# Kernel tuning notes

Hardware: AMD Instinct MI355X
Metric: run time of the kernel (lower is better)

The kernel has to match this reference:

```python
import jax, jax.numpy as jnp
from jax import lax
import numpy as np


def _lstm(x, h0, c0, Wih, Whh, bih, bhh):
    """Single-layer batch-first LSTM, PyTorch gate order (i, f, g, o).
    x: [B, T, I]; h0, c0: [B, H]. Returns (outputs [B, T, H], h_n [B, H], c_n [B, H])."""
    # Precompute input projections for all timesteps in one GEMM.
    xg = jnp.einsum('bti,gi->btg', x, Wih) + (bih + bhh)  # [B, T, 4H]
    H = h0.shape[-1]

    def step(carry, xt):
        h, c = carry
        gates = xt + h @ Whh.T  # [B, 4H]
        i, f, g, o = jnp.split(gates, 4, axis=-1)
        i = jax.nn.sigmoid(i)
        f = jax.nn.sigmoid(f)
        g = jnp.tanh(g)
        o = jax.nn.sigmoid(o)
        c = f * c + i * g
        h = o * jnp.tanh(c)
        return (h, c), h

    (h_n, c_n), hs = lax.scan(step, (h0, c0), jnp.swapaxes(xg, 0, 1))
    return jnp.swapaxes(hs, 0, 1), h_n, c_n


def setup_inputs() -> dict:
    key = jax.random.key(0)
    B, T, I, H, L = 4096, 512, 25, 20, 10
    ks = jax.random.split(key, 20)
    p = lambda k, shp: (jax.random.normal(k, shp, dtype=jnp.float32) * 0.1)
    return {
        'input_filters': jax.random.normal(ks[0], (B, T, I), dtype=jnp.float32),
        'h0': jnp.zeros((1, B, H), dtype=jnp.float32),
        'c0': jnp.zeros((1, B, H), dtype=jnp.float32),
        'noise': jax.random.normal(ks[1], (B, L), dtype=jnp.float32),
        'enc_Wih': p(ks[2], (4 * H, I)), 'enc_Whh': p(ks[3], (4 * H, H)),
        'enc_bih': p(ks[4], (4 * H,)), 'enc_bhh': p(ks[5], (4 * H,)),
        'dec_Wih': p(ks[6], (4 * H, I)), 'dec_Whh': p(ks[7], (4 * H, H)),
        'dec_bih': p(ks[8], (4 * H,)), 'dec_bhh': p(ks[9], (4 * H,)),
        'mean_W': p(ks[10], (L, H)), 'mean_b': p(ks[11], (L,)),
        'logvar_W': p(ks[12], (L, H)), 'logvar_b': p(ks[13], (L,)),
        'init_W': p(ks[14], (H, L)), 'init_b': p(ks[15], (H,)),
        'out_W': p(ks[16], (I, H)), 'out_b': p(ks[17], (I,)),
    }


def reference(input_filters, h0, c0, noise,
              enc_Wih, enc_Whh, enc_bih, enc_bhh,
              dec_Wih, dec_Whh, dec_bih, dec_bhh,
              mean_W, mean_b, logvar_W, logvar_b,
              init_W, init_b, out_W, out_b):
    # Encoder LSTM (num_layers == 1, squeeze the layer dim of h0/c0)
    _, h_n, c_n = _lstm(input_filters, h0[0], c0[0], enc_Wih, enc_Whh, enc_bih, enc_bhh)
    # mean / log_var from final hidden state, reparameterize
    mean = h_n @ mean_W.T + mean_b          # [B, L]
    log_var = h_n @ logvar_W.T + logvar_b   # [B, L]
    std = jnp.exp(0.5 * log_var)
    z = noise * std + mean                  # [B, L]
    # Decoder: z -> initial (h, c); teacher-forced decoder over same inputs
    hd = z @ init_W.T + init_b              # [B, H]
    out_dec, _, _ = _lstm(input_filters, hd, hd, dec_Wih, dec_Whh, dec_bih, dec_bhh)
    x_hat = jnp.einsum('bth,oh->bto', out_dec, out_W) + out_b  # [B, T, I]
    # Match torch shapes: mean/log_var/z carry num_layers leading dim
    return (x_hat, mean[None], log_var[None], z[None], h_n[None], c_n[None])
```

## Files before the change

### kernel.cpp

```cpp
#include <hip/hip_runtime.h>

#define NB 4096
#define NT 512
#define NI 25
#define NH 20
#define NL 10
#define CH 32

typedef float f4 __attribute__((ext_vector_type(4)));

#if __has_builtin(__builtin_amdgcn_rcpf)
__device__ __forceinline__ float rcpf(float x){ return __builtin_amdgcn_rcpf(x); }
#else
__device__ __forceinline__ float rcpf(float x){ return 1.0f/x; }
#endif

struct Smem {
  float xbuf[2][CH][32];
  float hbuf[2][32];
  float gbuf[2][128];
  float zbuf[2][12];
};

__device__ __forceinline__ void load_weights(
    const float* __restrict__ Wih, const float* __restrict__ Whh,
    const float* __restrict__ bih, const float* __restrict__ bhh,
    int p, int k, float (&w)[5][25], float (&bias)[5])
{
#pragma unroll
  for (int g=0; g<5; ++g){
    const int G = 5*k+g;
    if (p==0){
#pragma unroll
      for (int i=0;i<25;++i) w[g][i] = Wih[G*25+i];
      bias[g] = bih[G] + bhh[G];
    } else {
#pragma unroll
      for (int j=0;j<20;++j) w[g][j] = Whh[G*20+j];
#pragma unroll
      for (int j=20;j<25;++j) w[g][j] = 0.f;
      bias[g] = 0.f;
    }
  }
}

template<bool DEC>
__device__ __forceinline__ void lstm_loop(
    const float* __restrict__ xblk,
    Smem* sm, int lane, int r, int p, int k,
    const float (&w)[5][25], const float (&bias)[5],
    float& c,
    const float (&ow)[20], float obias,
    float* __restrict__ xhat)
{
  const bool is_g = ((k>>2)==2);
  const float gmul = is_g ? -2.0f : -1.0f;
  const bool upd = (p==0) || (k<4);
  const int  m   = (p==0) ? k : 16+k;
  const int  ai  = (m/5)*8 + (m%5);
  const int  q2  = lane & 31;
  const bool pj  = (q2 < 25);
  const float* opbase = (p==0) ? &sm->xbuf[r][0][0] : &sm->hbuf[r][0];

  for (int t=0; t<NT; ++t){
    const int tc = t & (CH-1);
    if (tc == 0){
      __syncthreads();
      const float* gsrc = xblk + (size_t)t*NI;
#pragma unroll
      for (int it=0; it<25; ++it){
        int idx = lane + it*64;
        int rr  = (idx >= 800) ? 1 : 0;
        int o   = idx - rr*800;
        int tt  = o / 25;
        int ii  = o - tt*25;
        sm->xbuf[rr][tt][ii] = gsrc[(size_t)rr*NT*NI + (size_t)tt*NI + ii];
      }
      __syncthreads();
    }

    const float* obp = (p==0) ? (opbase + tc*32) : opbase;
    float op[28];
#pragma unroll
    for (int v=0; v<7; ++v){
      f4 q = *(const f4*)(obp + 4*v);
      op[4*v+0]=q.x; op[4*v+1]=q.y; op[4*v+2]=q.z; op[4*v+3]=q.w;
    }

    float acc[5];
#pragma unroll
    for (int g=0; g<5; ++g) acc[g] = (p==0) ? bias[g] : 0.f;
#pragma unroll
    for (int i=0;i<25;++i){
      const float xv = op[i];
#pragma unroll
      for (int g=0;g<5;++g) acc[g] = fmaf(w[g][i], xv, acc[g]);
    }
#pragma unroll
    for (int g=0; g<5; ++g) acc[g] += __shfl_xor(acc[g], 16);

    float val[5];
#pragma unroll
    for (int g=0; g<5; ++g){
      float e = __expf(gmul*acc[g]);
      float s = rcpf(1.0f + e);
      val[g] = is_g ? (2.0f*s - 1.0f) : s;
    }
    if (p==0){
      f4 v4; v4.x=val[0]; v4.y=val[1]; v4.z=val[2]; v4.w=val[3];
      *(f4*)&sm->gbuf[r][k*8] = v4;
      sm->gbuf[r][k*8+4] = val[4];
    }
    __syncthreads();

    if (upd){
      float ig = sm->gbuf[r][ai];
      float fg = sm->gbuf[r][ai+32];
      float gg = sm->gbuf[r][ai+64];
      float og = sm->gbuf[r][ai+96];
      float cn = fmaf(fg, c, ig*gg);
      c = cn;
      float e  = __expf(-2.0f*cn);
      float th = 2.0f*rcpf(1.0f + e) - 1.0f;
      sm->hbuf[r][m] = og*th;
    }
    __syncthreads();

    if (DEC && pj){
      float h[20];
#pragma unroll
      for (int v=0; v<5; ++v){
        f4 q = *(const f4*)(&sm->hbuf[r][4*v]);
        h[4*v+0]=q.x; h[4*v+1]=q.y; h[4*v+2]=q.z; h[4*v+3]=q.w;
      }
      float a = obias;
#pragma unroll
      for (int j=0;j<20;++j) a = fmaf(ow[j], h[j], a);
      xhat[(size_t)t*NI] = a;
    }
  }
}

__global__ __launch_bounds__(64,2) void lstm_vae_kernel(
  const float* __restrict__ x, const float* __restrict__ h0, const float* __restrict__ c0,
  const float* __restrict__ noise,
  const float* __restrict__ eWih, const float* __restrict__ eWhh, const float* __restrict__ ebih, const float* __restrict__ ebhh,
  const float* __restrict__ dWih, const float* __restrict__ dWhh, const float* __restrict__ dbih, const float* __restrict__ dbhh,
  const float* __restrict__ mW, const float* __restrict__ mb,
  const float* __restrict__ lW, const float* __restrict__ lb,
  const float* __restrict__ iW, const float* __restrict__ ib,
  const float* __restrict__ oW, const float* __restrict__ ob,
  float* __restrict__ out)
{
  __shared__ Smem sm;
  const int lane = threadIdx.x;
  const int r = lane>>5, p = (lane>>4)&1, k = lane&15;
  const int b = blockIdx.x*2 + r;
  const bool upd = (p==0) || (k<4);
  const int  m   = (p==0) ? k : 16+k;
  const float* xblk = x + (size_t)(blockIdx.x*2)*NT*NI;

  ((float*)sm.hbuf)[lane] = 0.f;
  float c = 0.f;
  __syncthreads();
  if (upd){
    sm.hbuf[r][m] = h0[(size_t)b*NH + m];
    c = c0[(size_t)b*NH + m];
  }

  float w[5][25], bias[5];
  load_weights(eWih, eWhh, ebih, ebhh, p, k, w, bias);
  float ow[20]; float obias = 0.f;
#pragma unroll
  for (int j=0;j<20;++j) ow[j] = 0.f;
  __syncthreads();

  lstm_loop<false>(xblk, &sm, lane, r, p, k, w, bias, c, ow, obias, nullptr);
  __syncthreads();

  const size_t OFF1 = (size_t)NB*NT*NI;
  const size_t OFF2 = OFF1 + (size_t)NB*NL;
  const size_t OFF3 = OFF2 + (size_t)NB*NL;
  const size_t OFF4 = OFF3 + (size_t)NB*NL;
  const size_t OFF5 = OFF4 + (size_t)NB*NH;

  if (upd){
    out[OFF4 + (size_t)b*NH + m] = sm.hbuf[r][m];
    out[OFF5 + (size_t)b*NH + m] = c;
  }

  if (p==0 && k<10){
    float h[20];
#pragma unroll
    for (int j=0;j<20;++j) h[j] = sm.hbuf[r][j];
    float mm = mb[k], lv = lb[k];
#pragma unroll
    for (int j=0;j<20;++j){
      mm = fmaf(mW[k*20+j], h[j], mm);
      lv = fmaf(lW[k*20+j], h[j], lv);
    }
    float sd = __expf(0.5f*lv);
    float zz = fmaf(noise[(size_t)b*NL + k], sd, mm);
    out[OFF1 + (size_t)b*NL + k] = mm;
    out[OFF2 + (size_t)b*NL + k] = lv;
    out[OFF3 + (size_t)b*NL + k] = zz;
    sm.zbuf[r][k] = zz;
  }
  __syncthreads();

  if (upd){
    float hd = ib[m];
#pragma unroll
    for (int l=0;l<10;++l) hd = fmaf(iW[m*10+l], sm.zbuf[r][l], hd);
    c = hd;
    sm.hbuf[r][m] = hd;
  }

  load_weights(dWih, dWhh, dbih, dbhh, p, k, w, bias);
  const int q2 = lane & 31;
  if (q2 < 25){
#pragma unroll
    for (int j=0;j<20;++j) ow[j] = oW[q2*20+j];
    obias = ob[q2];
  }
  float* xhat = out + (size_t)b*NT*NI + q2;
  __syncthreads();

  lstm_loop<true>(xblk, &sm, lane, r, p, k, w, bias, c, ow, obias, xhat);
}

extern "C" void kernel_launch(void* const* d_in, const int* in_sizes, int n_in,
                              void* d_out, int out_size, void* d_ws, size_t ws_size,
                              hipStream_t stream) {
  const float* x     = (const float*)d_in[0];
  const float* h0    = (const float*)d_in[1];
  const float* c0    = (const float*)d_in[2];
  const float* noise = (const float*)d_in[3];
  const float* eWih  = (const float*)d_in[4];
  const float* eWhh  = (const float*)d_in[5];
  const float* ebih  = (const float*)d_in[6];
  const float* ebhh  = (const float*)d_in[7];
  const float* dWih  = (const float*)d_in[8];
  const float* dWhh  = (const float*)d_in[9];
  const float* dbih  = (const float*)d_in[10];
  const float* dbhh  = (const float*)d_in[11];
  const float* mW    = (const float*)d_in[12];
  const float* mb    = (const float*)d_in[13];
  const float* lW    = (const float*)d_in[14];
  const float* lb    = (const float*)d_in[15];
  const float* iW    = (const float*)d_in[16];
  const float* ib    = (const float*)d_in[17];
  const float* oW    = (const float*)d_in[18];
  const float* ob    = (const float*)d_in[19];
  float* out = (float*)d_out;

  hipLaunchKernelGGL(lstm_vae_kernel, dim3(NB/2), dim3(64), 0, stream,
                     x, h0, c0, noise,
                     eWih, eWhh, ebih, ebhh,
                     dWih, dWhh, dbih, dbhh,
                     mW, mb, lW, lb, iW, ib, oW, ob, out);
}
```

Baseline: 1.032 ms.

## Map one batch row per block, split gate dot products across four lane groups

Each 64-thread block now handles a single batch row instead of two. The 45-element [x;h] dot product per gate is split across four 16-lane quarters of 12 weights each and combined with two xor shuffles. This cuts per-thread weight registers from 125 to 60 and raises launch bounds to allow four blocks per CU, so the serial per-timestep chain gets shorter and occupancy goes up. In exchange the grid doubles, and there are more shuffles, more barriers per unit of work and redundant activation math.

```diff
diff --git a/kernel.cpp b/kernel.cpp
--- a/kernel.cpp
+++ b/kernel.cpp
@@ -16,29 +16,38 @@
 #endif
 
 struct Smem {
-  float xbuf[2][CH][32];
-  float hbuf[2][32];
-  float gbuf[2][128];
-  float zbuf[2][12];
+  float xbuf[CH][28];
+  float hbuf[24];
+  float gbuf[132];
+  float zbuf[12];
 };
 
 __device__ __forceinline__ void load_weights(
     const float* __restrict__ Wih, const float* __restrict__ Whh,
     const float* __restrict__ bih, const float* __restrict__ bhh,
-    int p, int k, float (&w)[5][25], float (&bias)[5])
+    int p, int k, float (&w)[5][12], float (&bias)[5])
 {
 #pragma unroll
   for (int g=0; g<5; ++g){
     const int G = 5*k+g;
+    const float* wi = Wih + G*25;
+    const float* wh = Whh + G*20;
     if (p==0){
 #pragma unroll
-      for (int i=0;i<25;++i) w[g][i] = Wih[G*25+i];
+      for (int j=0;j<12;++j) w[g][j] = wi[j];
       bias[g] = bih[G] + bhh[G];
+    } else if (p==1){
+#pragma unroll
+      for (int j=0;j<12;++j) w[g][j] = wi[12+j];
+      bias[g] = 0.f;
+    } else if (p==2){
+      w[g][0]=wi[24]; w[g][1]=0.f; w[g][2]=0.f; w[g][3]=0.f;
+#pragma unroll
+      for (int j=0;j<8;++j) w[g][4+j] = wh[j];
+      bias[g] = 0.f;
     } else {
 #pragma unroll
-      for (int j=0;j<20;++j) w[g][j] = Whh[G*20+j];
-#pragma unroll
-      for (int j=20;j<25;++j) w[g][j] = 0.f;
+      for (int j=0;j<12;++j) w[g][j] = wh[8+j];
       bias[g] = 0.f;
     }
   }
@@ -46,102 +55,99 @@
 
 template<bool DEC>
 __device__ __forceinline__ void lstm_loop(
-    const float* __restrict__ xblk,
-    Smem* sm, int lane, int r, int p, int k,
-    const float (&w)[5][25], const float (&bias)[5],
-    float& c,
+    const float* __restrict__ xrow,
+    Smem* sm, int lane, int p, int k,
+    const float (&w)[5][12], const float (&bias)[5], float& c,
     const float (&ow)[20], float obias,
     float* __restrict__ xhat)
 {
   const bool is_g = ((k>>2)==2);
   const float gmul = is_g ? -2.0f : -1.0f;
-  const bool upd = (p==0) || (k<4);
-  const int  m   = (p==0) ? k : 16+k;
-  const int  ai  = (m/5)*8 + (m%5);
-  const int  q2  = lane & 31;
-  const bool pj  = (q2 < 25);
-  const float* opbase = (p==0) ? &sm->xbuf[r][0][0] : &sm->hbuf[r][0];
+  const int lin = lane;
+  const int ai  = (lin/5)*8 + (lin%5);
+  const float* xb0 = &sm->xbuf[0][0];
+  const float* hb  = &sm->hbuf[0];
+  const float* b1 = (p==3) ? hb+8  : xb0 + 12*p;
+  const float* b2 = (p< 2) ? xb0 + 4 + 12*p : ((p==2) ? hb+0  : hb+12);
+  const float* b3 = (p< 2) ? xb0 + 8 + 12*p : ((p==2) ? hb+4  : hb+16);
+  const int m1  = (p<3) ? ~0 : 0;
+  const int m23 = (p<2) ? ~0 : 0;
 
   for (int t=0; t<NT; ++t){
     const int tc = t & (CH-1);
     if (tc == 0){
       __syncthreads();
-      const float* gsrc = xblk + (size_t)t*NI;
-#pragma unroll
-      for (int it=0; it<25; ++it){
+      const float* gsrc = xrow + (size_t)t*NI;
+#pragma unroll
+      for (int it=0; it<14; ++it){
         int idx = lane + it*64;
-        int rr  = (idx >= 800) ? 1 : 0;
-        int o   = idx - rr*800;
-        int tt  = o / 25;
-        int ii  = o - tt*25;
-        sm->xbuf[rr][tt][ii] = gsrc[(size_t)rr*NT*NI + (size_t)tt*NI + ii];
+        int tt = idx/28, ii = idx - tt*28;
+        sm->xbuf[tt][ii] = (ii < NI) ? gsrc[tt*NI + ii] : 0.f;
       }
       __syncthreads();
     }
-
-    const float* obp = (p==0) ? (opbase + tc*32) : opbase;
-    float op[28];
-#pragma unroll
-    for (int v=0; v<7; ++v){
-      f4 q = *(const f4*)(obp + 4*v);
-      op[4*v+0]=q.x; op[4*v+1]=q.y; op[4*v+2]=q.z; op[4*v+3]=q.w;
-    }
+    const int off = tc*28;
+    f4 v1 = *(const f4*)(b1 + (off & m1));
+    f4 v2 = *(const f4*)(b2 + (off & m23));
+    f4 v3 = *(const f4*)(b3 + (off & m23));
 
     float acc[5];
 #pragma unroll
-    for (int g=0; g<5; ++g) acc[g] = (p==0) ? bias[g] : 0.f;
-#pragma unroll
-    for (int i=0;i<25;++i){
-      const float xv = op[i];
-#pragma unroll
-      for (int g=0;g<5;++g) acc[g] = fmaf(w[g][i], xv, acc[g]);
-    }
-#pragma unroll
-    for (int g=0; g<5; ++g) acc[g] += __shfl_xor(acc[g], 16);
-
-    float val[5];
+    for (int g=0; g<5; ++g) acc[g] = bias[g];
 #pragma unroll
     for (int g=0; g<5; ++g){
-      float e = __expf(gmul*acc[g]);
-      float s = rcpf(1.0f + e);
-      val[g] = is_g ? (2.0f*s - 1.0f) : s;
+      acc[g]=fmaf(w[g][0] ,v1.x,acc[g]); acc[g]=fmaf(w[g][1] ,v1.y,acc[g]);
+      acc[g]=fmaf(w[g][2] ,v1.z,acc[g]); acc[g]=fmaf(w[g][3] ,v1.w,acc[g]);
+      acc[g]=fmaf(w[g][4] ,v2.x,acc[g]); acc[g]=fmaf(w[g][5] ,v2.y,acc[g]);
+      acc[g]=fmaf(w[g][6] ,v2.z,acc[g]); acc[g]=fmaf(w[g][7] ,v2.w,acc[g]);
+      acc[g]=fmaf(w[g][8] ,v3.x,acc[g]); acc[g]=fmaf(w[g][9] ,v3.y,acc[g]);
+      acc[g]=fmaf(w[g][10],v3.z,acc[g]); acc[g]=fmaf(w[g][11],v3.w,acc[g]);
+    }
+#pragma unroll
+    for (int g=0; g<5; ++g){
+      acc[g] += __shfl_xor(acc[g], 16);
+      acc[g] += __shfl_xor(acc[g], 32);
     }
     if (p==0){
-      f4 v4; v4.x=val[0]; v4.y=val[1]; v4.z=val[2]; v4.w=val[3];
-      *(f4*)&sm->gbuf[r][k*8] = v4;
-      sm->gbuf[r][k*8+4] = val[4];
+      float val[5];
+#pragma unroll
+      for (int g=0; g<5; ++g){
+        float e = __expf(gmul*acc[g]);
+        float s = rcpf(1.0f + e);
+        val[g] = is_g ? (2.0f*s - 1.0f) : s;
+      }
+      f4 v; v.x=val[0]; v.y=val[1]; v.z=val[2]; v.w=val[3];
+      *(f4*)&sm->gbuf[k*8] = v;
+      sm->gbuf[k*8+4] = val[4];
     }
     __syncthreads();
-
-    if (upd){
-      float ig = sm->gbuf[r][ai];
-      float fg = sm->gbuf[r][ai+32];
-      float gg = sm->gbuf[r][ai+64];
-      float og = sm->gbuf[r][ai+96];
+    if (lin < NH){
+      float ig = sm->gbuf[ai];
+      float fg = sm->gbuf[ai+32];
+      float gg = sm->gbuf[ai+64];
+      float og = sm->gbuf[ai+96];
       float cn = fmaf(fg, c, ig*gg);
       c = cn;
       float e  = __expf(-2.0f*cn);
       float th = 2.0f*rcpf(1.0f + e) - 1.0f;
-      sm->hbuf[r][m] = og*th;
+      sm->hbuf[lin] = og*th;
     }
     __syncthreads();
-
-    if (DEC && pj){
-      float h[20];
-#pragma unroll
-      for (int v=0; v<5; ++v){
-        f4 q = *(const f4*)(&sm->hbuf[r][4*v]);
-        h[4*v+0]=q.x; h[4*v+1]=q.y; h[4*v+2]=q.z; h[4*v+3]=q.w;
-      }
+    if (DEC && lin < NI){
+      f4 h0_=*(const f4*)(hb+0),  h1_=*(const f4*)(hb+4),  h2_=*(const f4*)(hb+8);
+      f4 h3_=*(const f4*)(hb+12), h4_=*(const f4*)(hb+16);
       float a = obias;
-#pragma unroll
-      for (int j=0;j<20;++j) a = fmaf(ow[j], h[j], a);
-      xhat[(size_t)t*NI] = a;
-    }
-  }
-}
-
-__global__ __launch_bounds__(64,2) void lstm_vae_kernel(
+      a=fmaf(ow[0] ,h0_.x,a); a=fmaf(ow[1] ,h0_.y,a); a=fmaf(ow[2] ,h0_.z,a); a=fmaf(ow[3] ,h0_.w,a);
+      a=fmaf(ow[4] ,h1_.x,a); a=fmaf(ow[5] ,h1_.y,a); a=fmaf(ow[6] ,h1_.z,a); a=fmaf(ow[7] ,h1_.w,a);
+      a=fmaf(ow[8] ,h2_.x,a); a=fmaf(ow[9] ,h2_.y,a); a=fmaf(ow[10],h2_.z,a); a=fmaf(ow[11],h2_.w,a);
+      a=fmaf(ow[12],h3_.x,a); a=fmaf(ow[13],h3_.y,a); a=fmaf(ow[14],h3_.z,a); a=fmaf(ow[15],h3_.w,a);
+      a=fmaf(ow[16],h4_.x,a); a=fmaf(ow[17],h4_.y,a); a=fmaf(ow[18],h4_.z,a); a=fmaf(ow[19],h4_.w,a);
+      xhat[(size_t)t*NI + lin] = a;
+    }
+  }
+}
+
+__global__ __launch_bounds__(64,4) void lstm_vae_kernel(
   const float* __restrict__ x, const float* __restrict__ h0, const float* __restrict__ c0,
   const float* __restrict__ noise,
   const float* __restrict__ eWih, const float* __restrict__ eWhh, const float* __restrict__ ebih, const float* __restrict__ ebhh,
@@ -154,29 +160,25 @@
 {
   __shared__ Smem sm;
   const int lane = threadIdx.x;
-  const int r = lane>>5, p = (lane>>4)&1, k = lane&15;
-  const int b = blockIdx.x*2 + r;
-  const bool upd = (p==0) || (k<4);
-  const int  m   = (p==0) ? k : 16+k;
-  const float* xblk = x + (size_t)(blockIdx.x*2)*NT*NI;
-
-  ((float*)sm.hbuf)[lane] = 0.f;
+  const int p = lane>>4, k = lane&15, lin = lane;
+  const int b = blockIdx.x;
+  const float* xrow = x + (size_t)b*NT*NI;
+
+  float w[5][12], bias[5];
+  float ow[20]; float obias = 0.f;
+#pragma unroll
+  for (int j=0;j<20;++j) ow[j] = 0.f;
   float c = 0.f;
+
+  if (lin < NH){
+    sm.hbuf[lin] = h0[(size_t)b*NH + lin];
+    c = c0[(size_t)b*NH + lin];
+  }
+  if (lin >= NH && lin < 24) sm.hbuf[lin] = 0.f;
+  load_weights(eWih, eWhh, ebih, ebhh, p, k, w, bias);
   __syncthreads();
-  if (upd){
-    sm.hbuf[r][m] = h0[(size_t)b*NH + m];
-    c = c0[(size_t)b*NH + m];
-  }
-
-  float w[5][25], bias[5];
-  load_weights(eWih, eWhh, ebih, ebhh, p, k, w, bias);
-  float ow[20]; float obias = 0.f;
-#pragma unroll
-  for (int j=0;j<20;++j) ow[j] = 0.f;
-  __syncthreads();
-
-  lstm_loop<false>(xblk, &sm, lane, r, p, k, w, bias, c, ow, obias, nullptr);
-  __syncthreads();
+
+  lstm_loop<false>(xrow, &sm, lane, p, k, w, bias, c, ow, obias, nullptr);
 
   const size_t OFF1 = (size_t)NB*NT*NI;
   const size_t OFF2 = OFF1 + (size_t)NB*NL;
@@ -184,49 +186,45 @@
   const size_t OFF4 = OFF3 + (size_t)NB*NL;
   const size_t OFF5 = OFF4 + (size_t)NB*NH;
 
-  if (upd){
-    out[OFF4 + (size_t)b*NH + m] = sm.hbuf[r][m];
-    out[OFF5 + (size_t)b*NH + m] = c;
-  }
-
-  if (p==0 && k<10){
+  if (lin < NH){
+    out[OFF4 + (size_t)b*NH + lin] = sm.hbuf[lin];
+    out[OFF5 + (size_t)b*NH + lin] = c;
+  }
+  if (lin < NL){
     float h[20];
 #pragma unroll
-    for (int j=0;j<20;++j) h[j] = sm.hbuf[r][j];
-    float mm = mb[k], lv = lb[k];
+    for (int j=0;j<20;++j) h[j] = sm.hbuf[j];
+    float mm = mb[lin], lv = lb[lin];
 #pragma unroll
     for (int j=0;j<20;++j){
-      mm = fmaf(mW[k*20+j], h[j], mm);
-      lv = fmaf(lW[k*20+j], h[j], lv);
+      mm = fmaf(mW[lin*20+j], h[j], mm);
+      lv = fmaf(lW[lin*20+j], h[j], lv);
     }
     float sd = __expf(0.5f*lv);
-    float zz = fmaf(noise[(size_t)b*NL + k], sd, mm);
-    out[OFF1 + (size_t)b*NL + k] = mm;
-    out[OFF2 + (size_t)b*NL + k] = lv;
-    out[OFF3 + (size_t)b*NL + k] = zz;
-    sm.zbuf[r][k] = zz;
+    float zz = fmaf(noise[(size_t)b*NL + lin], sd, mm);
+    out[OFF1 + (size_t)b*NL + lin] = mm;
+    out[OFF2 + (size_t)b*NL + lin] = lv;
+    out[OFF3 + (size_t)b*NL + lin] = zz;
+    sm.zbuf[lin] = zz;
   }
   __syncthreads();
-
-  if (upd){
-    float hd = ib[m];
-#pragma unroll
-    for (int l=0;l<10;++l) hd = fmaf(iW[m*10+l], sm.zbuf[r][l], hd);
+  if (lin < NH){
+    float hd = ib[lin];
+#pragma unroll
+    for (int l=0;l<NL;++l) hd = fmaf(iW[lin*NL+l], sm.zbuf[l], hd);
     c = hd;
-    sm.hbuf[r][m] = hd;
-  }
-
+    sm.hbuf[lin] = hd;
+  }
   load_weights(dWih, dWhh, dbih, dbhh, p, k, w, bias);
-  const int q2 = lane & 31;
-  if (q2 < 25){
-#pragma unroll
-    for (int j=0;j<20;++j) ow[j] = oW[q2*20+j];
-    obias = ob[q2];
-  }
-  float* xhat = out + (size_t)b*NT*NI + q2;
+  if (lin < NI){
+#pragma unroll
+    for (int j=0;j<20;++j) ow[j] = oW[lin*20+j];
+    obias = ob[lin];
+  }
   __syncthreads();
 
-  lstm_loop<true>(xblk, &sm, lane, r, p, k, w, bias, c, ow, obias, xhat);
+  lstm_loop<true>(xrow, &sm, lane, p, k, w, bias, c, ow, obias,
+                  out + (size_t)b*NT*NI);
 }
 
 extern "C" void kernel_launch(void* const* d_in, const int* in_sizes, int n_in,
@@ -254,7 +252,7 @@
   const float* ob    = (const float*)d_in[19];
   float* out = (float*)d_out;
 
-  hipLaunchKernelGGL(lstm_vae_kernel, dim3(NB/2), dim3(64), 0, stream,
+  hipLaunchKernelGGL(lstm_vae_kernel, dim3(NB), dim3(64), 0, stream,
                      x, h0, c0, noise,
                      eWih, eWhh, ebih, ebhh,
                      dWih, dWhh, dbih, dbhh,
```

Measured after the change: 1.562 ms. 1.51x slower.
